# Performance work log

Hardware: AMD Instinct MI355X
Metric: run time of the kernel (lower is better)

## Reference

```python
import jax, jax.numpy as jnp
import numpy as np

N_HEAD = 16
D_K = 64
D_MODEL = N_HEAD * D_K
LN_EPS = 1e-5


def setup_inputs() -> dict:
    key = jax.random.key(0)
    ks = jax.random.split(key, 11)
    B, Tq, Tk = 4, 2048, 2048
    s = 1.0 / np.sqrt(D_MODEL)
    return {
        "q": jax.random.normal(ks[0], (B, Tq, D_MODEL), jnp.float32),
        "k": jax.random.normal(ks[1], (B, Tk, D_MODEL), jnp.float32),
        "v": jax.random.normal(ks[2], (B, Tk, D_MODEL), jnp.float32),
        "Wq": jax.random.normal(ks[3], (D_MODEL, D_MODEL), jnp.float32) * s,
        "bq": jnp.zeros((D_MODEL,), jnp.float32),
        "Wk": jax.random.normal(ks[4], (D_MODEL, D_MODEL), jnp.float32) * s,
        "bk": jnp.zeros((D_MODEL,), jnp.float32),
        "Wv": jax.random.normal(ks[5], (D_MODEL, D_MODEL), jnp.float32) * s,
        "bv": jnp.zeros((D_MODEL,), jnp.float32),
        "Wo": jax.random.normal(ks[6], (D_MODEL, D_MODEL), jnp.float32) * s,
        "bo": jnp.zeros((D_MODEL,), jnp.float32),
        "gamma": jnp.ones((D_MODEL,), jnp.float32),
        "beta": jnp.zeros((D_MODEL,), jnp.float32),
    }


def reference(q, k, v, Wq, bq, Wk, bk, Wv, bv, Wo, bo, gamma, beta):
    B, Tq, _ = q.shape
    Tk = k.shape[1]
    temperature = jnp.asarray(D_K ** 0.5, q.dtype)

    # projections (torch Linear: x @ W.T + b), reshape to heads: [B, T, H, DK]
    qh = (q @ Wq.T + bq).reshape(B, Tq, N_HEAD, D_K)
    kh = (k @ Wk.T + bk).reshape(B, Tk, N_HEAD, D_K)
    vh = (v @ Wv.T + bv).reshape(B, Tk, N_HEAD, D_K)

    # scores [B, H, Tq, Tk]; softmax over Tk (dropout is identity in eval)
    scores = jnp.einsum('bqhd,bkhd->bhqk', qh, kh) / temperature
    attn = jax.nn.softmax(scores, axis=-1)

    # attention output -> concat heads [B, Tq, D_MODEL]
    out = jnp.einsum('bhqk,bkhd->bqhd', attn, vh).reshape(B, Tq, D_MODEL)

    out = out @ Wo.T + bo
    x = out + q  # residual
    mu = jnp.mean(x, axis=-1, keepdims=True)
    var = jnp.var(x, axis=-1, keepdims=True)
    out_norm = (x - mu) * jax.lax.rsqrt(var + LN_EPS) * gamma + beta

    # attn returned in torch layout [NHead*B, Tq, Tk]
    attn_flat = attn.transpose(1, 0, 2, 3).reshape(N_HEAD * B, Tq, Tk)
    return (out_norm, attn_flat)
```

## Files before the change

kernel.cpp:

```cpp
#include <hip/hip_runtime.h>
#include <cstdint>
#include <cstddef>

typedef __attribute__((ext_vector_type(4))) float f32x4;
typedef __attribute__((ext_vector_type(8))) short s16x8;
typedef __attribute__((ext_vector_type(8))) _Float16 f16x8;
typedef __attribute__((ext_vector_type(4))) unsigned short u16x4;
typedef __attribute__((ext_vector_type(8))) unsigned short u16x8;

#define MFMA_BF16(a, b, c) __builtin_amdgcn_mfma_f32_16x16x32_bf16((a), (b), (c), 0, 0, 0)
#define MFMA_F16(a, b, c) __builtin_amdgcn_mfma_f32_16x16x32_f16((a), (b), (c), 0, 0, 0)
#define GLOAD_LDS16(src, dst)                                             \
  __builtin_amdgcn_global_load_lds(                                       \
      (const __attribute__((address_space(1))) void*)(src),               \
      (__attribute__((address_space(3))) void*)(dst), 16, 0, 0)

static constexpr int kD = 1024;
static constexpr int kT = 2048;

__device__ __forceinline__ unsigned short f2bf(float f) {
  union { float f; uint32_t u; } v; v.f = f;
  uint32_t r = v.u + 0x7fffu + ((v.u >> 16) & 1u);
  return (unsigned short)(r >> 16);
}
__device__ __forceinline__ unsigned short f2h(float f) {
  union { _Float16 h; unsigned short u; } cv;
  cv.h = (_Float16)f;
  return cv.u;
}

__global__ __launch_bounds__(256) void convert_all_k(
    const float* __restrict__ q, const float* __restrict__ k,
    const float* __restrict__ v, const float* __restrict__ Wq,
    const float* __restrict__ Wk, const float* __restrict__ Wv,
    const float* __restrict__ Wo, unsigned short* __restrict__ q_h,
    unsigned short* __restrict__ k_h, unsigned short* __restrict__ v_b,
    unsigned short* __restrict__ Wq_h, unsigned short* __restrict__ Wk_h,
    unsigned short* __restrict__ Wv_b, unsigned short* __restrict__ Wo_b) {
  constexpr int nq4 = (4 * 2048 * 1024) / 4;
  constexpr int nw4 = (1024 * 1024) / 4;
  constexpr int total = 3 * nq4 + 4 * nw4;
  for (int i = blockIdx.x * 256 + threadIdx.x; i < total; i += gridDim.x * 256) {
    const float* src;
    unsigned short* dst;
    int off;
    bool use_f16;
    if (i < nq4) { src = q; dst = q_h; off = i; use_f16 = true; }
    else if (i < 2 * nq4) { src = k; dst = k_h; off = i - nq4; use_f16 = true; }
    else if (i < 3 * nq4) { src = v; dst = v_b; off = i - 2 * nq4; use_f16 = false; }
    else if (i < 3 * nq4 + nw4) { src = Wq; dst = Wq_h; off = i - 3 * nq4; use_f16 = true; }
    else if (i < 3 * nq4 + 2 * nw4) { src = Wk; dst = Wk_h; off = i - 3 * nq4 - nw4; use_f16 = true; }
    else if (i < 3 * nq4 + 3 * nw4) { src = Wv; dst = Wv_b; off = i - 3 * nq4 - 2 * nw4; use_f16 = false; }
    else { src = Wo; dst = Wo_b; off = i - 3 * nq4 - 3 * nw4; use_f16 = false; }
    f32x4 vv = ((const f32x4*)src)[off];
    u16x4 o4;
#pragma unroll
    for (int j = 0; j < 4; j++) o4[j] = use_f16 ? f2h(vv[j]) : f2bf(vv[j]);
    ((u16x4*)dst)[off] = o4;
  }
}

template <int MODE>
__global__ __launch_bounds__(256, 3) void gemm_16(
    const unsigned short* __restrict__ X, const unsigned short* __restrict__ W,
    const float* __restrict__ bias, const float* __restrict__ resid,
    unsigned short* __restrict__ outB, float* __restrict__ outF, float oscale) {
  __shared__ unsigned short smem[MODE == 1 ? 16640 : 16384];
  unsigned short* Ah = smem;
  unsigned short* Bh = smem + 8192;

  const int tid = threadIdx.x, lane = tid & 63, w = tid >> 6;
  const int wg = (blockIdx.x & 7) * 64 + (blockIdx.x >> 3);
  const int m0 = (wg >> 3) * 128, n0 = (wg & 7) * 128;
  const int wm0 = (w >> 1) * 64, wn0 = (w & 1) * 64;
  const int lr = lane & 15, lk = lane >> 4;
  const int srow = lane >> 3, sslot = (lane & 7) ^ srow;

  const size_t xoff = (size_t)(m0 + w * 32 + srow) * kD + sslot * 8;
  const size_t woff = (size_t)(n0 + w * 32 + srow) * kD + sslot * 8;

  f32x4 acc[4][4];
#pragma unroll
  for (int i = 0; i < 4; i++)
#pragma unroll
    for (int j = 0; j < 4; j++) acc[i][j] = (f32x4){0.f, 0.f, 0.f, 0.f};

  for (int kt = 0; kt < kD / 64; ++kt) {
    __syncthreads();
    const int kof = kt * 64;
#pragma unroll
    for (int i = 0; i < 4; i++) {
      const int ldst = (w * 32 + i * 8) * 64;
      GLOAD_LDS16(X + xoff + (size_t)i * 8 * kD + kof, &Ah[ldst]);
      GLOAD_LDS16(W + woff + (size_t)i * 8 * kD + kof, &Bh[ldst]);
    }
    __syncthreads();
#pragma unroll
    for (int ks = 0; ks < 2; ks++) {
      s16x8 af[4], bf[4];
#pragma unroll
      for (int i = 0; i < 4; i++) {
        const int ra = wm0 + i * 16 + lr;
        const int oa = ra * 128 + ((((ks * 4) + lk) ^ (ra & 7)) << 4);
        const int rb = wn0 + i * 16 + lr;
        const int ob = rb * 128 + ((((ks * 4) + lk) ^ (rb & 7)) << 4);
        af[i] = *(const s16x8*)((const char*)Ah + oa);
        bf[i] = *(const s16x8*)((const char*)Bh + ob);
      }
#pragma unroll
      for (int i = 0; i < 4; i++)
#pragma unroll
        for (int j = 0; j < 4; j++) {
          if constexpr (MODE == 0) {
            acc[i][j] = MFMA_F16(*(const f16x8*)&af[i], *(const f16x8*)&bf[j],
                                 acc[i][j]);
          } else {
            acc[i][j] = MFMA_BF16(af[i], bf[j], acc[i][j]);
          }
        }
    }
  }

  if constexpr (MODE == 1) {
    __syncthreads();
#pragma unroll
    for (int j = 0; j < 4; j++) {
      const int col = wn0 + j * 16 + lr;
      const float bv = bias[n0 + col];
#pragma unroll
      for (int i = 0; i < 4; i++)
#pragma unroll
        for (int r = 0; r < 4; r++) {
          const int row = wm0 + i * 16 + lk * 4 + r;
          smem[col * 130 + row] = f2bf(acc[i][j][r] + bv);
        }
    }
    __syncthreads();
    const int b = m0 >> 11, t0 = m0 & 2047;
    const int dl = tid >> 1, th = (tid & 1) * 64;
    const int h = (n0 + dl) >> 6, dh = (n0 + dl) & 63;
    unsigned short* dst = outB + ((size_t)((b * 16 + h) * 64 + dh)) * kT + t0 + th;
#pragma unroll
    for (int i = 0; i < 8; i++) {
      u16x8 o = *(const u16x8*)&smem[dl * 130 + th + i * 8];
      *(u16x8*)(dst + i * 8) = o;
    }
    return;
  }

#pragma unroll
  for (int j = 0; j < 4; j++) {
    const int col = n0 + wn0 + j * 16 + lr;
    const float bv = bias[col];
#pragma unroll
    for (int i = 0; i < 4; i++)
#pragma unroll
      for (int r = 0; r < 4; r++) {
        const int row = m0 + wm0 + i * 16 + lk * 4 + r;
        const size_t idx = (size_t)row * kD + col;
        float vv = acc[i][j][r] + bv;
        if constexpr (MODE == 0) {
          outB[idx] = f2h(vv * oscale);
        } else {
          outF[idx] = vv + resid[idx];
        }
      }
  }
}

__global__ __launch_bounds__(256, 3) void attn_fused(
    const unsigned short* __restrict__ qh, const unsigned short* __restrict__ kh,
    const unsigned short* __restrict__ vhT, unsigned short* __restrict__ attn_out,
    float* __restrict__ attn_p) {
  __shared__ unsigned short kbuf[2][64 * 64];
  __shared__ unsigned short vbuf[2][64 * 64];
  __shared__ unsigned short qp[9216];

  const int tid = threadIdx.x, lane = tid & 63, w = tid >> 6;
  const int lr = lane & 15, lk = lane >> 4;
  const int srow = lane >> 3, sslot = (lane & 7) ^ srow;
  const int wg = (blockIdx.x & 7) * 128 + (blockIdx.x >> 3);
  const int bh = wg >> 4, qt = wg & 15;
  const int h = bh >> 2, b = bh & 3;
  const int q0 = qt * 128, qm0 = w * 32;

  const size_t qsrc = (size_t)(b * kT + q0 + w * 32 + srow) * kD + h * 64 + sslot * 8;
#pragma unroll
  for (int i = 0; i < 4; i++)
    GLOAD_LDS16(qh + qsrc + (size_t)i * 8 * kD, &qp[(w * 32 + i * 8) * 64]);

  const size_t kbase = (size_t)(b * kT + w * 16 + srow) * kD + h * 64 + sslot * 8;
  const size_t vbase = ((size_t)((b * 16 + h) * 64) + w * 16 + srow) * kT + sslot * 8;

#pragma unroll
  for (int i = 0; i < 2; i++) {
    const int ldst = (w * 16 + i * 8) * 64;
    GLOAD_LDS16(kh + kbase + (size_t)(i * 8) * kD, &kbuf[0][ldst]);
    GLOAD_LDS16(vhT + vbase + (size_t)i * 8 * kT, &vbuf[0][ldst]);
  }
  __syncthreads();

  f16x8 qf[2][2];
#pragma unroll
  for (int mq = 0; mq < 2; mq++)
#pragma unroll
    for (int ks = 0; ks < 2; ks++) {
      const int rq = qm0 + mq * 16 + lr;
      qf[mq][ks] = *(const f16x8*)((const char*)qp + rq * 128 +
                                   ((((ks * 4) + lk) ^ (rq & 7)) << 4));
    }

  float l_part[2] = {0.f, 0.f};
  f32x4 pv[2][4];
#pragma unroll
  for (int mq = 0; mq < 2; mq++)
#pragma unroll
    for (int nd = 0; nd < 4; nd++) pv[mq][nd] = (f32x4){0.f, 0.f, 0.f, 0.f};
  unsigned short* p_w = &qp[w * 2304];

  for (int kt = 0; kt < kT / 64; ++kt) {
    if (kt + 1 < kT / 64) {
#pragma unroll
      for (int i = 0; i < 2; i++) {
        const int ldst = (w * 16 + i * 8) * 64;
        GLOAD_LDS16(kh + kbase + (size_t)((kt + 1) * 64 + i * 8) * kD,
                    &kbuf[(kt + 1) & 1][ldst]);
        GLOAD_LDS16(vhT + vbase + (size_t)i * 8 * kT + (kt + 1) * 64,
                    &vbuf[(kt + 1) & 1][ldst]);
      }
    }
    const unsigned short* kb = kbuf[kt & 1];
    const unsigned short* vb = vbuf[kt & 1];
    f32x4 sc[2][4];
#pragma unroll
    for (int mq = 0; mq < 2; mq++)
#pragma unroll
      for (int ni = 0; ni < 4; ni++) sc[mq][ni] = (f32x4){0.f, 0.f, 0.f, 0.f};
#pragma unroll
    for (int ks = 0; ks < 2; ks++) {
      f16x8 kf[4];
#pragma unroll
      for (int ni = 0; ni < 4; ni++) {
        const int rk = ni * 16 + lr;
        kf[ni] = *(const f16x8*)((const char*)kb + rk * 128 +
                                 ((((ks * 4) + lk) ^ (rk & 7)) << 4));
      }
#pragma unroll
      for (int mq = 0; mq < 2; mq++)
#pragma unroll
        for (int ni = 0; ni < 4; ni++)
          sc[mq][ni] = MFMA_F16(kf[ni], qf[mq][ks], sc[mq][ni]);
    }
#pragma unroll
    for (int mq = 0; mq < 2; mq++) {
#pragma unroll
      for (int ni = 0; ni < 4; ni++) {
        f32x4 pr;
#pragma unroll
        for (int r = 0; r < 4; r++) pr[r] = __expf(sc[mq][ni][r]);
        l_part[mq] += pr[0] + pr[1] + pr[2] + pr[3];
        uint32_t d0, d1;
        asm("v_cvt_pk_bf16_f32 %0, %1, %2" : "=v"(d0) : "v"(pr[0]), "v"(pr[1]));
        asm("v_cvt_pk_bf16_f32 %0, %1, %2" : "=v"(d1) : "v"(pr[2]), "v"(pr[3]));
        uint2 dd; dd.x = d0; dd.y = d1;
        *(uint2*)&p_w[(mq * 16 + lr) * 72 + ni * 16 + 4 * lk] = dd;
      }
    }
#pragma unroll
    for (int ks = 0; ks < 2; ks++) {
      s16x8 pf[2], vf[4];
#pragma unroll
      for (int mq = 0; mq < 2; mq++)
        pf[mq] = *(const s16x8*)&p_w[(mq * 16 + lr) * 72 + ks * 32 + lk * 8];
#pragma unroll
      for (int nd = 0; nd < 4; nd++) {
        const int row = nd * 16 + lr;
        const int sw2 = ((ks * 4) + lk) ^ (row & 7);
        vf[nd] = *(const s16x8*)((const char*)vb + row * 128 + (sw2 << 4));
      }
#pragma unroll
      for (int mq = 0; mq < 2; mq++)
#pragma unroll
        for (int nd = 0; nd < 4; nd++)
          pv[mq][nd] = MFMA_BF16(pf[mq], vf[nd], pv[mq][nd]);
    }
    __syncthreads();
  }

  float rl[2];
#pragma unroll
  for (int mq = 0; mq < 2; mq++) {
    float s = l_part[mq];
    s += __shfl_xor(s, 16, 64);
    s += __shfl_xor(s, 32, 64);
    rl[mq] = 1.0f / s;
  }
#pragma unroll
  for (int mq = 0; mq < 2; mq++)
#pragma unroll
    for (int r = 0; r < 4; r++) {
      const int qloc = lk * 4 + r;
      const float rlq = __shfl(rl[mq], qloc, 64);
#pragma unroll
      for (int nd = 0; nd < 4; nd++) {
        const int qrow = q0 + qm0 + mq * 16 + qloc;
        attn_out[((size_t)(b * kT + qrow)) * kD + h * 64 + nd * 16 + lr] =
            f2bf(pv[mq][nd][r] * rlq);
      }
    }

#pragma unroll
  for (int i = 0; i < 2; i++)
    GLOAD_LDS16(kh + kbase + (size_t)(i * 8) * kD, &kbuf[0][(w * 16 + i * 8) * 64]);
  __syncthreads();

  for (int kt = 0; kt < kT / 64; ++kt) {
    if (kt + 1 < kT / 64) {
#pragma unroll
      for (int i = 0; i < 2; i++)
        GLOAD_LDS16(kh + kbase + (size_t)((kt + 1) * 64 + i * 8) * kD,
                    &kbuf[(kt + 1) & 1][(w * 16 + i * 8) * 64]);
    }
    const unsigned short* kb = kbuf[kt & 1];
    f32x4 sc[2][4];
#pragma unroll
    for (int mq = 0; mq < 2; mq++)
#pragma unroll
      for (int ni = 0; ni < 4; ni++) sc[mq][ni] = (f32x4){0.f, 0.f, 0.f, 0.f};
#pragma unroll
    for (int ks = 0; ks < 2; ks++) {
      f16x8 kf[4];
#pragma unroll
      for (int ni = 0; ni < 4; ni++) {
        const int rk = ni * 16 + lr;
        kf[ni] = *(const f16x8*)((const char*)kb + rk * 128 +
                                 ((((ks * 4) + lk) ^ (rk & 7)) << 4));
      }
#pragma unroll
      for (int mq = 0; mq < 2; mq++)
#pragma unroll
        for (int ni = 0; ni < 4; ni++)
          sc[mq][ni] = MFMA_F16(kf[ni], qf[mq][ks], sc[mq][ni]);
    }
#pragma unroll
    for (int mq = 0; mq < 2; mq++) {
      const int qrow = q0 + qm0 + mq * 16 + lr;
      float* prow = attn_p + ((size_t)(bh * kT + qrow)) * kT + kt * 64 + 4 * lk;
#pragma unroll
      for (int ni = 0; ni < 4; ni++) {
        f32x4 pr;
#pragma unroll
        for (int r = 0; r < 4; r++) pr[r] = __expf(sc[mq][ni][r]) * rl[mq];
        __builtin_nontemporal_store(pr, (f32x4*)(prow + ni * 16));
      }
    }
    __syncthreads();
  }
}

__global__ __launch_bounds__(256) void ln_kernel(
    const float* __restrict__ x, const float* __restrict__ gamma,
    const float* __restrict__ beta, float* __restrict__ out) {
  __shared__ float ssum[4], ssq[4];
  const int row = blockIdx.x, tid = threadIdx.x;
  f32x4 v = *(const f32x4*)&x[(size_t)row * kD + tid * 4];
  float s = v[0] + v[1] + v[2] + v[3];
  float q2 = v[0] * v[0] + v[1] * v[1] + v[2] * v[2] + v[3] * v[3];
#pragma unroll
  for (int d = 1; d < 64; d <<= 1) {
    s += __shfl_xor(s, d, 64);
    q2 += __shfl_xor(q2, d, 64);
  }
  const int w = tid >> 6, lane = tid & 63;
  if (lane == 0) {
    ssum[w] = s;
    ssq[w] = q2;
  }
  __syncthreads();
  s = ssum[0] + ssum[1] + ssum[2] + ssum[3];
  q2 = ssq[0] + ssq[1] + ssq[2] + ssq[3];
  const float mu = s * (1.f / 1024.f);
  const float var = q2 * (1.f / 1024.f) - mu * mu;
  const float rstd = rsqrtf(var + 1e-5f);
  f32x4 g = *(const f32x4*)&gamma[tid * 4];
  f32x4 bb = *(const f32x4*)&beta[tid * 4];
  f32x4 o;
#pragma unroll
  for (int j = 0; j < 4; j++) o[j] = (v[j] - mu) * rstd * g[j] + bb[j];
  *(f32x4*)&out[(size_t)row * kD + tid * 4] = o;
}

extern "C" void kernel_launch(void* const* d_in, const int* in_sizes, int n_in,
                              void* d_out, int out_size, void* d_ws,
                              size_t ws_size, hipStream_t stream) {
  const float* q = (const float*)d_in[0];
  const float* k = (const float*)d_in[1];
  const float* v = (const float*)d_in[2];
  const float* Wq = (const float*)d_in[3];
  const float* bq = (const float*)d_in[4];
  const float* Wk = (const float*)d_in[5];
  const float* bk = (const float*)d_in[6];
  const float* Wv = (const float*)d_in[7];
  const float* bv = (const float*)d_in[8];
  const float* Wo = (const float*)d_in[9];
  const float* bo = (const float*)d_in[10];
  const float* gamma = (const float*)d_in[11];
  const float* beta = (const float*)d_in[12];

  float* out = (float*)d_out;
  float* attn_p = out + (size_t)8192 * 1024;

  constexpr size_t NQ = (size_t)4 * 2048 * 1024;
  constexpr size_t NW = (size_t)1024 * 1024;

  unsigned short* w16 = (unsigned short*)d_ws;
  unsigned short* q_h  = w16 + 0 * NQ;
  unsigned short* k_h  = w16 + 1 * NQ;
  unsigned short* v_b  = w16 + 2 * NQ;
  unsigned short* qh_h = w16 + 3 * NQ;
  unsigned short* kh_h = w16 + 4 * NQ;
  unsigned short* vhT  = w16 + 5 * NQ;
  unsigned short* ao_b = w16 + 6 * NQ;
  unsigned short* Wq_h = w16 + 7 * NQ;
  unsigned short* Wk_h = Wq_h + NW;
  unsigned short* Wv_b = Wq_h + 2 * NW;
  unsigned short* Wo_b = Wq_h + 3 * NW;
  float* xbuf = (float*)(Wq_h + 4 * NW);

  dim3 blk(256);
  convert_all_k<<<2048, blk, 0, stream>>>(q, k, v, Wq, Wk, Wv, Wo, q_h, k_h,
                                          v_b, Wq_h, Wk_h, Wv_b, Wo_b);

  gemm_16<0><<<512, blk, 0, stream>>>(q_h, Wq_h, bq, nullptr, qh_h, nullptr,
                                      0.125f);
  gemm_16<0><<<512, blk, 0, stream>>>(k_h, Wk_h, bk, nullptr, kh_h, nullptr,
                                      1.0f);
  gemm_16<1><<<512, blk, 0, stream>>>(v_b, Wv_b, bv, nullptr, vhT, nullptr,
                                      1.0f);
  attn_fused<<<1024, blk, 0, stream>>>(qh_h, kh_h, vhT, ao_b, attn_p);
  gemm_16<2><<<512, blk, 0, stream>>>(ao_b, Wo_b, bo, q, nullptr, xbuf, 1.0f);
  ln_kernel<<<8192, blk, 0, stream>>>(xbuf, gamma, beta, out);
}
```

Measured before the change: 509.4 us.

## Process two query tiles per attention block, overlapping one tile's probability write with the other's PV pass

Each attention workgroup now handles two 128-row query tiles (X and Y) and the grid is halved. After the normal softmax/PV pass for tile X, a merged loop streams K/V once, writing tile X's normalized probabilities while computing tile Y's row sums and PV product. A final pass writes tile Y's probabilities. This removes one of the three K sweeps per tile pair and interleaves the store-bound probability writes with MFMA-heavy work. In exchange it uses more registers (occupancy hint drops from 3 to 2) and launches half as many blocks.

```diff
diff --git a/kernel.cpp b/kernel.cpp
--- a/kernel.cpp
+++ b/kernel.cpp
@@ -168,7 +168,7 @@
   }
 }
 
-__global__ __launch_bounds__(256, 3) void attn_fused(
+__global__ __launch_bounds__(256, 2) void attn_fused2(
     const unsigned short* __restrict__ qh, const unsigned short* __restrict__ kh,
     const unsigned short* __restrict__ vhT, unsigned short* __restrict__ attn_out,
     float* __restrict__ attn_p) {
@@ -179,44 +179,51 @@
   const int tid = threadIdx.x, lane = tid & 63, w = tid >> 6;
   const int lr = lane & 15, lk = lane >> 4;
   const int srow = lane >> 3, sslot = (lane & 7) ^ srow;
-  const int wg = (blockIdx.x & 7) * 128 + (blockIdx.x >> 3);
-  const int bh = wg >> 4, qt = wg & 15;
+  const int wg = (blockIdx.x & 7) * 64 + (blockIdx.x >> 3);
+  const int bh = wg >> 3, p = wg & 7;
   const int h = bh >> 2, b = bh & 3;
-  const int q0 = qt * 128, qm0 = w * 32;
-
-  const size_t qsrc = (size_t)(b * kT + q0 + w * 32 + srow) * kD + h * 64 + sslot * 8;
-#pragma unroll
-  for (int i = 0; i < 4; i++)
-    GLOAD_LDS16(qh + qsrc + (size_t)i * 8 * kD, &qp[(w * 32 + i * 8) * 64]);
-
+  const int q0X = p * 128, q0Y = (p + 8) * 128;
+  const int qm0 = w * 32;
+
+  const size_t qsrcX = (size_t)(b * kT + q0X + w * 32 + srow) * kD + h * 64 + sslot * 8;
+  const size_t qsrcY = (size_t)(b * kT + q0Y + w * 32 + srow) * kD + h * 64 + sslot * 8;
+  unsigned short* vflat = &vbuf[0][0];
+#pragma unroll
+  for (int i = 0; i < 4; i++) {
+    GLOAD_LDS16(qh + qsrcX + (size_t)i * 8 * kD, &qp[(w * 32 + i * 8) * 64]);
+    GLOAD_LDS16(qh + qsrcY + (size_t)i * 8 * kD, &vflat[(w * 32 + i * 8) * 64]);
+  }
   const size_t kbase = (size_t)(b * kT + w * 16 + srow) * kD + h * 64 + sslot * 8;
   const size_t vbase = ((size_t)((b * 16 + h) * 64) + w * 16 + srow) * kT + sslot * 8;
-
-#pragma unroll
-  for (int i = 0; i < 2; i++) {
-    const int ldst = (w * 16 + i * 8) * 64;
-    GLOAD_LDS16(kh + kbase + (size_t)(i * 8) * kD, &kbuf[0][ldst]);
-    GLOAD_LDS16(vhT + vbase + (size_t)i * 8 * kT, &vbuf[0][ldst]);
-  }
+#pragma unroll
+  for (int i = 0; i < 2; i++)
+    GLOAD_LDS16(kh + kbase + (size_t)(i * 8) * kD, &kbuf[0][(w * 16 + i * 8) * 64]);
   __syncthreads();
 
-  f16x8 qf[2][2];
+  f16x8 qfX[2][2], qfY[2][2];
 #pragma unroll
   for (int mq = 0; mq < 2; mq++)
 #pragma unroll
     for (int ks = 0; ks < 2; ks++) {
       const int rq = qm0 + mq * 16 + lr;
-      qf[mq][ks] = *(const f16x8*)((const char*)qp + rq * 128 +
-                                   ((((ks * 4) + lk) ^ (rq & 7)) << 4));
-    }
-
+      const int off = rq * 128 + ((((ks * 4) + lk) ^ (rq & 7)) << 4);
+      qfX[mq][ks] = *(const f16x8*)((const char*)qp + off);
+      qfY[mq][ks] = *(const f16x8*)((const char*)vflat + off);
+    }
+  __syncthreads();
+
+#pragma unroll
+  for (int i = 0; i < 2; i++)
+    GLOAD_LDS16(vhT + vbase + (size_t)i * 8 * kT, &vbuf[0][(w * 16 + i * 8) * 64]);
+  __syncthreads();
+
+  unsigned short* p_w = &qp[w * 2304];
   float l_part[2] = {0.f, 0.f};
   f32x4 pv[2][4];
 #pragma unroll
   for (int mq = 0; mq < 2; mq++)
 #pragma unroll
     for (int nd = 0; nd < 4; nd++) pv[mq][nd] = (f32x4){0.f, 0.f, 0.f, 0.f};
-  unsigned short* p_w = &qp[w * 2304];
 
   for (int kt = 0; kt < kT / 64; ++kt) {
     if (kt + 1 < kT / 64) {
@@ -249,7 +256,7 @@
       for (int mq = 0; mq < 2; mq++)
 #pragma unroll
         for (int ni = 0; ni < 4; ni++)
-          sc[mq][ni] = MFMA_F16(kf[ni], qf[mq][ks], sc[mq][ni]);
+          sc[mq][ni] = MFMA_F16(kf[ni], qfX[mq][ks], sc[mq][ni]);
     }
 #pragma unroll
     for (int mq = 0; mq < 2; mq++) {
@@ -287,23 +294,166 @@
     __syncthreads();
   }
 
-  float rl[2];
+  float rlX[2];
 #pragma unroll
   for (int mq = 0; mq < 2; mq++) {
     float s = l_part[mq];
     s += __shfl_xor(s, 16, 64);
     s += __shfl_xor(s, 32, 64);
-    rl[mq] = 1.0f / s;
+    rlX[mq] = 1.0f / s;
   }
 #pragma unroll
   for (int mq = 0; mq < 2; mq++)
 #pragma unroll
     for (int r = 0; r < 4; r++) {
       const int qloc = lk * 4 + r;
-      const float rlq = __shfl(rl[mq], qloc, 64);
+      const float rlq = __shfl(rlX[mq], qloc, 64);
 #pragma unroll
       for (int nd = 0; nd < 4; nd++) {
-        const int qrow = q0 + qm0 + mq * 16 + qloc;
+        const int qrow = q0X + qm0 + mq * 16 + qloc;
+        attn_out[((size_t)(b * kT + qrow)) * kD + h * 64 + nd * 16 + lr] =
+            f2bf(pv[mq][nd][r] * rlq);
+      }
+    }
+
+  l_part[0] = 0.f; l_part[1] = 0.f;
+#pragma unroll
+  for (int mq = 0; mq < 2; mq++)
+#pragma unroll
+    for (int nd = 0; nd < 4; nd++) pv[mq][nd] = (f32x4){0.f, 0.f, 0.f, 0.f};
+
+#pragma unroll
+  for (int i = 0; i < 2; i++) {
+    const int ldst = (w * 16 + i * 8) * 64;
+    GLOAD_LDS16(kh + kbase + (size_t)(i * 8) * kD, &kbuf[0][ldst]);
+    GLOAD_LDS16(vhT + vbase + (size_t)i * 8 * kT, &vbuf[0][ldst]);
+  }
+  __syncthreads();
+
+  for (int kt = 0; kt < kT / 64; ++kt) {
+    if (kt + 1 < kT / 64) {
+#pragma unroll
+      for (int i = 0; i < 2; i++) {
+        const int ldst = (w * 16 + i * 8) * 64;
+        GLOAD_LDS16(kh + kbase + (size_t)((kt + 1) * 64 + i * 8) * kD,
+                    &kbuf[(kt + 1) & 1][ldst]);
+        GLOAD_LDS16(vhT + vbase + (size_t)i * 8 * kT + (kt + 1) * 64,
+                    &vbuf[(kt + 1) & 1][ldst]);
+      }
+    }
+    const unsigned short* kb = kbuf[kt & 1];
+    const unsigned short* vb = vbuf[kt & 1];
+
+    {
+      f32x4 sc[2][4];
+#pragma unroll
+      for (int mq = 0; mq < 2; mq++)
+#pragma unroll
+        for (int ni = 0; ni < 4; ni++) sc[mq][ni] = (f32x4){0.f, 0.f, 0.f, 0.f};
+#pragma unroll
+      for (int ks = 0; ks < 2; ks++) {
+        f16x8 kf[4];
+#pragma unroll
+        for (int ni = 0; ni < 4; ni++) {
+          const int rk = ni * 16 + lr;
+          kf[ni] = *(const f16x8*)((const char*)kb + rk * 128 +
+                                   ((((ks * 4) + lk) ^ (rk & 7)) << 4));
+        }
+#pragma unroll
+        for (int mq = 0; mq < 2; mq++)
+#pragma unroll
+          for (int ni = 0; ni < 4; ni++)
+            sc[mq][ni] = MFMA_F16(kf[ni], qfX[mq][ks], sc[mq][ni]);
+      }
+#pragma unroll
+      for (int mq = 0; mq < 2; mq++) {
+        const int qrow = q0X + qm0 + mq * 16 + lr;
+        float* prow = attn_p + ((size_t)(bh * kT + qrow)) * kT + kt * 64 + 4 * lk;
+#pragma unroll
+        for (int ni = 0; ni < 4; ni++) {
+          f32x4 pr;
+#pragma unroll
+          for (int r = 0; r < 4; r++) pr[r] = __expf(sc[mq][ni][r]) * rlX[mq];
+          __builtin_nontemporal_store(pr, (f32x4*)(prow + ni * 16));
+        }
+      }
+    }
+
+    {
+      f32x4 sc[2][4];
+#pragma unroll
+      for (int mq = 0; mq < 2; mq++)
+#pragma unroll
+        for (int ni = 0; ni < 4; ni++) sc[mq][ni] = (f32x4){0.f, 0.f, 0.f, 0.f};
+#pragma unroll
+      for (int ks = 0; ks < 2; ks++) {
+        f16x8 kf[4];
+#pragma unroll
+        for (int ni = 0; ni < 4; ni++) {
+          const int rk = ni * 16 + lr;
+          kf[ni] = *(const f16x8*)((const char*)kb + rk * 128 +
+                                   ((((ks * 4) + lk) ^ (rk & 7)) << 4));
+        }
+#pragma unroll
+        for (int mq = 0; mq < 2; mq++)
+#pragma unroll
+          for (int ni = 0; ni < 4; ni++)
+            sc[mq][ni] = MFMA_F16(kf[ni], qfY[mq][ks], sc[mq][ni]);
+      }
+#pragma unroll
+      for (int mq = 0; mq < 2; mq++) {
+#pragma unroll
+        for (int ni = 0; ni < 4; ni++) {
+          f32x4 pr;
+#pragma unroll
+          for (int r = 0; r < 4; r++) pr[r] = __expf(sc[mq][ni][r]);
+          l_part[mq] += pr[0] + pr[1] + pr[2] + pr[3];
+          uint32_t d0, d1;
+          asm("v_cvt_pk_bf16_f32 %0, %1, %2" : "=v"(d0) : "v"(pr[0]), "v"(pr[1]));
+          asm("v_cvt_pk_bf16_f32 %0, %1, %2" : "=v"(d1) : "v"(pr[2]), "v"(pr[3]));
+          uint2 dd; dd.x = d0; dd.y = d1;
+          *(uint2*)&p_w[(mq * 16 + lr) * 72 + ni * 16 + 4 * lk] = dd;
+        }
+      }
+#pragma unroll
+      for (int ks = 0; ks < 2; ks++) {
+        s16x8 pf[2], vf[4];
+#pragma unroll
+        for (int mq = 0; mq < 2; mq++)
+          pf[mq] = *(const s16x8*)&p_w[(mq * 16 + lr) * 72 + ks * 32 + lk * 8];
+#pragma unroll
+        for (int nd = 0; nd < 4; nd++) {
+          const int row = nd * 16 + lr;
+          const int sw2 = ((ks * 4) + lk) ^ (row & 7);
+          vf[nd] = *(const s16x8*)((const char*)vb + row * 128 + (sw2 << 4));
+        }
+#pragma unroll
+        for (int mq = 0; mq < 2; mq++)
+#pragma unroll
+          for (int nd = 0; nd < 4; nd++)
+            pv[mq][nd] = MFMA_BF16(pf[mq], vf[nd], pv[mq][nd]);
+      }
+    }
+    __syncthreads();
+  }
+
+  float rlY[2];
+#pragma unroll
+  for (int mq = 0; mq < 2; mq++) {
+    float s = l_part[mq];
+    s += __shfl_xor(s, 16, 64);
+    s += __shfl_xor(s, 32, 64);
+    rlY[mq] = 1.0f / s;
+  }
+#pragma unroll
+  for (int mq = 0; mq < 2; mq++)
+#pragma unroll
+    for (int r = 0; r < 4; r++) {
+      const int qloc = lk * 4 + r;
+      const float rlq = __shfl(rlY[mq], qloc, 64);
+#pragma unroll
+      for (int nd = 0; nd < 4; nd++) {
+        const int qrow = q0Y + qm0 + mq * 16 + qloc;
         attn_out[((size_t)(b * kT + qrow)) * kD + h * 64 + nd * 16 + lr] =
             f2bf(pv[mq][nd][r] * rlq);
       }
@@ -340,17 +490,17 @@
       for (int mq = 0; mq < 2; mq++)
 #pragma unroll
         for (int ni = 0; ni < 4; ni++)
-          sc[mq][ni] = MFMA_F16(kf[ni], qf[mq][ks], sc[mq][ni]);
+          sc[mq][ni] = MFMA_F16(kf[ni], qfY[mq][ks], sc[mq][ni]);
     }
 #pragma unroll
     for (int mq = 0; mq < 2; mq++) {
-      const int qrow = q0 + qm0 + mq * 16 + lr;
+      const int qrow = q0Y + qm0 + mq * 16 + lr;
       float* prow = attn_p + ((size_t)(bh * kT + qrow)) * kT + kt * 64 + 4 * lk;
 #pragma unroll
       for (int ni = 0; ni < 4; ni++) {
         f32x4 pr;
 #pragma unroll
-        for (int r = 0; r < 4; r++) pr[r] = __expf(sc[mq][ni][r]) * rl[mq];
+        for (int r = 0; r < 4; r++) pr[r] = __expf(sc[mq][ni][r]) * rlY[mq];
         __builtin_nontemporal_store(pr, (f32x4*)(prow + ni * 16));
       }
     }
@@ -437,7 +587,7 @@
                                       1.0f);
   gemm_16<1><<<512, blk, 0, stream>>>(v_b, Wv_b, bv, nullptr, vhT, nullptr,
                                       1.0f);
-  attn_fused<<<1024, blk, 0, stream>>>(qh_h, kh_h, vhT, ao_b, attn_p);
+  attn_fused2<<<512, blk, 0, stream>>>(qh_h, kh_h, vhT, ao_b, attn_p);
   gemm_16<2><<<512, blk, 0, stream>>>(ao_b, Wo_b, bo, q, nullptr, xbuf, 1.0f);
   ln_kernel<<<8192, blk, 0, stream>>>(xbuf, gamma, beta, out);
 }
```

New measurement: 615.1 us. 1.21x slower.
